# Performance work log

Hardware: AMD Instinct MI355X
Metric: run time of the kernel (lower is better)

## Reference

```python
import jax, jax.numpy as jnp
import numpy as np

B = 64          # number of scenes/graphs
OBJS = 2048     # objects per scene
N = B * OBJS    # total objects
D = 256         # representation_dim
K = 2           # num_channels


def setup_inputs() -> dict:
    key = jax.random.key(0)
    k1, k2, k3 = jax.random.split(key, 3)
    x_aggregation = jax.random.normal(k1, (N, D), dtype=jnp.float32)
    num_objs = jnp.full((B,), OBJS, dtype=jnp.int32)
    # glorot for att_shared [1, D]: fan_in + fan_out = 1 + D
    std_shared = float(np.sqrt(6.0 / (1 + D)))
    att_shared = jax.random.uniform(k2, (1, D), dtype=jnp.float32,
                                    minval=-std_shared, maxval=std_shared)
    # glorot for att_scale [K, 1]
    std_scale = float(np.sqrt(6.0 / (K + 1)))
    att_scale = jax.random.uniform(k3, (K, 1), dtype=jnp.float32,
                                   minval=-std_scale, maxval=std_scale)
    channel_bias = jnp.zeros((K, D), dtype=jnp.float32)
    return {"x_aggregation": x_aggregation, "num_objs": num_objs,
            "att_shared": att_shared, "att_scale": att_scale,
            "channel_bias": channel_bias}


def reference(x_aggregation, num_objs, att_shared, att_scale, channel_bias):
    batch_idx = jnp.repeat(jnp.arange(B), num_objs, total_repeat_length=N)  # [N]
    # scatter_mean: per-scene context features [B, D]
    seg_sum = jax.ops.segment_sum(x_aggregation, batch_idx, num_segments=B)
    counts = jnp.maximum(num_objs, 1).astype(x_aggregation.dtype)
    ctx = seg_sum / counts[:, None]
    attn_in = jax.nn.leaky_relu(x_aggregation + ctx[batch_idx], negative_slope=0.2)  # [N, D]
    # per-channel logits: ((attn_in + bias[k]) . att_shared) * scale[k]
    base = attn_in @ att_shared[0]                 # [N]
    bias_term = channel_bias @ att_shared[0]       # [K]
    logits = (base[:, None] + bias_term[None, :]) * att_scale[:, 0][None, :]  # [N, K]
    # per-channel segment softmax over objects within each scene
    m = jax.ops.segment_max(logits, batch_idx, num_segments=B)   # [B, K]
    z = jnp.exp(logits - m[batch_idx])
    s = jax.ops.segment_sum(z, batch_idx, num_segments=B)        # [B, K]
    attn_weights = z / s[batch_idx]                              # [N, K]
    # attention-weighted pooling per channel -> [B, D, K]
    weighted = x_aggregation[:, :, None] * attn_weights[:, None, :]  # [N, D, K]
    scene_features = jax.ops.segment_sum(weighted, batch_idx, num_segments=B)
    return scene_features, attn_weights
```

## Files before the change

### kernel.cpp

```cpp
#include <hip/hip_runtime.h>

#define B    64
#define OBJS 2048
#define NTOT (B * OBJS)
#define D    256
#define K    2

#define NBLK 256
#define BPS  4
#define CHF  (OBJS / BPS)
#define RPWF (CHF / 4)

#define S1   16
#define CH   (OBJS / S1)
#define RPW  (CH / 4)

#define WS_P1  0
#define WS_UP  (1024 * 256)
#define WS_ZP  (WS_UP + 1024 * 512)
#define WS_E   (WS_ZP + 1024 * 8)
#define WS_CNT (WS_E + NTOT * 2)

static __device__ __forceinline__ float lrelu02(float v) {
    return v > 0.0f ? v : 0.2f * v;
}

__global__ __launch_bounds__(256, 1) void fused_all(
        const float* __restrict__ x,
        const int* __restrict__ num_objs,
        const float* __restrict__ att_scale,
        const float* __restrict__ att_shared,
        const float* __restrict__ channel_bias,
        float* __restrict__ ws,
        float* __restrict__ out) {
    extern __shared__ float4 xbuf4[];
    __shared__ float pl[4 * 576];
    __shared__ float esm[4 * 16];
    __shared__ float sctx[D];
    __shared__ float sbt[2];
    __shared__ int   sfin;

    int blk = blockIdx.x;
    int b = blk / BPS;
    int t = threadIdx.x;
    int w = t >> 6, l = t & 63;
    int r = l & 7, sl = l >> 3;
    int row0 = blk * CHF + w * RPWF;
    int* cntA = (int*)(ws + WS_CNT);
    int* cntF = cntA + B;

    float4 kp[10][8];
    float4* xw = xbuf4 + (size_t)w * (32 * 64);
    const float* px = x + (size_t)row0 * D + 4 * l;

    float4 acc = make_float4(0.f, 0.f, 0.f, 0.f);
#pragma unroll
    for (int g = 0; g < 10; ++g) {
#pragma unroll
        for (int j = 0; j < 8; ++j) {
            float4 v = *(const float4*)(px + (size_t)(g * 8 + j) * D);
            kp[g][j] = v;
            acc.x += v.x; acc.y += v.y; acc.z += v.z; acc.w += v.w;
        }
    }
#pragma unroll
    for (int gl = 0; gl < 32; ++gl) {
        float4 v = *(const float4*)(px + (size_t)(80 + gl) * D);
        xw[gl * 64 + l] = v;
        acc.x += v.x; acc.y += v.y; acc.z += v.z; acc.w += v.w;
    }
#pragma unroll
    for (int j = 0; j < 16; ++j) {
        float4 v = *(const float4*)(px + (size_t)(112 + j) * D);
        acc.x += v.x; acc.y += v.y; acc.z += v.z; acc.w += v.w;
    }
    *(float4*)(pl + w * D + 4 * l) = acc;
    __syncthreads();
    if (t < 64) {
        float4 a = ((const float4*)(pl        ))[t];
        float4 e = ((const float4*)(pl +     D))[t];
        float4 f = ((const float4*)(pl + 2 * D))[t];
        float4 g = ((const float4*)(pl + 3 * D))[t];
        float4 s4 = make_float4(a.x + e.x + f.x + g.x, a.y + e.y + f.y + g.y,
                                a.z + e.z + f.z + g.z, a.w + e.w + f.w + g.w);
        *(float4*)(ws + WS_P1 + blk * D + 4 * t) = s4;
    }
    __syncthreads();
    if (t == 0) {
        __threadfence();
        atomicAdd(&cntA[b], 1);
        while (__hip_atomic_load(&cntA[b], __ATOMIC_RELAXED,
                                 __HIP_MEMORY_SCOPE_AGENT) < BPS)
            __builtin_amdgcn_s_sleep(2);
        __threadfence();
    }
    __syncthreads();

    {
        int cnt = num_objs[b]; if (cnt < 1) cnt = 1;
        float inv = 1.0f / (float)cnt;
        float sum = 0.f;
#pragma unroll
        for (int c = 0; c < BPS; ++c) sum += ws[WS_P1 + (b * BPS + c) * D + t];
        sctx[t] = sum * inv;
    }
    if (t < 64) {
        float4 a = ((const float4*)att_shared)[t];
#pragma unroll
        for (int k = 0; k < K; ++k) {
            float4 cb = ((const float4*)(channel_bias + k * D))[t];
            float v = a.x * cb.x + a.y * cb.y + a.z * cb.z + a.w * cb.w;
#pragma unroll
            for (int m = 32; m > 0; m >>= 1) v += __shfl_xor(v, m);
            if (t == 0) sbt[k] = v;
        }
    }
    __syncthreads();

    float4 a4   = ((const float4*)att_shared)[l];
    float4 ctx4 = *(const float4*)(sctx + 4 * l);
    float bt0 = sbt[0], bt1 = sbt[1];
    float s0 = att_scale[0], s1 = att_scale[1];

    float4 acc0 = make_float4(0.f, 0.f, 0.f, 0.f);
    float4 acc1 = make_float4(0.f, 0.f, 0.f, 0.f);
    float z0 = 0.f, z1 = 0.f;
    float e0c = 0.f, e1c = 0.f;
    float e0d = 0.f, e1d = 0.f;
    float* pw = pl  + w * 576;
    float* ew = esm + w * 16;

#define PD(V) (lrelu02((V).x + ctx4.x) * a4.x + lrelu02((V).y + ctx4.y) * a4.y \
             + lrelu02((V).z + ctx4.z) * a4.z + lrelu02((V).w + ctx4.w) * a4.w)
#define ACC(V, EA, EB) { acc0.x += (V).x * (EA); acc0.y += (V).y * (EA);      \
                         acc0.z += (V).z * (EA); acc0.w += (V).w * (EA);      \
                         acc1.x += (V).x * (EB); acc1.y += (V).y * (EB);      \
                         acc1.z += (V).z * (EB); acc1.w += (V).w * (EB); }
#define PROC_GROUP(GI, L0, L1, L2, L3, L4, L5, L6, L7) {                      \
    pw[l * 9 + 0] = PD(L0); pw[l * 9 + 1] = PD(L1);                           \
    pw[l * 9 + 2] = PD(L2); pw[l * 9 + 3] = PD(L3);                           \
    pw[l * 9 + 4] = PD(L4); pw[l * 9 + 5] = PD(L5);                           \
    pw[l * 9 + 6] = PD(L6); pw[l * 9 + 7] = PD(L7);                           \
    float tr = 0.f;                                                           \
    _Pragma("unroll")                                                         \
    for (int q = 0; q < 8; ++q) tr += pw[(sl * 8 + q) * 9 + r];               \
    tr += __shfl_xor(tr, 8);                                                  \
    tr += __shfl_xor(tr, 16);                                                 \
    tr += __shfl_xor(tr, 32);                                                 \
    float e0 = __expf((tr + bt0) * s0);                                       \
    float e1 = __expf((tr + bt1) * s1);                                       \
    if ((GI) == (l >> 3))     { e0c = e0; e1c = e1; }                         \
    if ((GI) == 8 + (l >> 3)) { e0d = e0; e1d = e1; }                         \
    if (l < 8) { ew[2 * l] = e0; ew[2 * l + 1] = e1; }                        \
    float4 E0 = *(const float4*)(ew + 0);                                     \
    float4 E1 = *(const float4*)(ew + 4);                                     \
    float4 E2 = *(const float4*)(ew + 8);                                     \
    float4 E3 = *(const float4*)(ew + 12);                                    \
    z0 += E0.x + E0.z + E1.x + E1.z + E2.x + E2.z + E3.x + E3.z;              \
    z1 += E0.y + E0.w + E1.y + E1.w + E2.y + E2.w + E3.y + E3.w;              \
    ACC(L0, E0.x, E0.y) ACC(L1, E0.z, E0.w)                                   \
    ACC(L2, E1.x, E1.y) ACC(L3, E1.z, E1.w)                                   \
    ACC(L4, E2.x, E2.y) ACC(L5, E2.z, E2.w)                                   \
    ACC(L6, E3.x, E3.y) ACC(L7, E3.z, E3.w)                                   \
}
#define PG_KP(G) PROC_GROUP(G, kp[G][0], kp[G][1], kp[G][2], kp[G][3],        \
                               kp[G][4], kp[G][5], kp[G][6], kp[G][7])

    PG_KP(0) PG_KP(1) PG_KP(2) PG_KP(3)
    float4 sa[8], sb[8];
#pragma unroll
    for (int j = 0; j < 8; ++j) sa[j] = *(const float4*)(px + (size_t)(112 + j) * D);
#pragma unroll
    for (int j = 0; j < 8; ++j) sb[j] = *(const float4*)(px + (size_t)(120 + j) * D);

    PG_KP(4) PG_KP(5) PG_KP(6) PG_KP(7) PG_KP(8) PG_KP(9)
    {
        float4 q0 = xw[0 * 64 + l], q1 = xw[1 * 64 + l], q2 = xw[2 * 64 + l],
               q3 = xw[3 * 64 + l], q4 = xw[4 * 64 + l], q5 = xw[5 * 64 + l],
               q6 = xw[6 * 64 + l], q7 = xw[7 * 64 + l];
        PROC_GROUP(10, q0, q1, q2, q3, q4, q5, q6, q7)
    }
    {
        float4 q0 = xw[8 * 64 + l], q1 = xw[9 * 64 + l], q2 = xw[10 * 64 + l],
               q3 = xw[11 * 64 + l], q4 = xw[12 * 64 + l], q5 = xw[13 * 64 + l],
               q6 = xw[14 * 64 + l], q7 = xw[15 * 64 + l];
        PROC_GROUP(11, q0, q1, q2, q3, q4, q5, q6, q7)
    }
    {
        float4 q0 = xw[16 * 64 + l], q1 = xw[17 * 64 + l], q2 = xw[18 * 64 + l],
               q3 = xw[19 * 64 + l], q4 = xw[20 * 64 + l], q5 = xw[21 * 64 + l],
               q6 = xw[22 * 64 + l], q7 = xw[23 * 64 + l];
        PROC_GROUP(12, q0, q1, q2, q3, q4, q5, q6, q7)
    }
    {
        float4 q0 = xw[24 * 64 + l], q1 = xw[25 * 64 + l], q2 = xw[26 * 64 + l],
               q3 = xw[27 * 64 + l], q4 = xw[28 * 64 + l], q5 = xw[29 * 64 + l],
               q6 = xw[30 * 64 + l], q7 = xw[31 * 64 + l];
        PROC_GROUP(13, q0, q1, q2, q3, q4, q5, q6, q7)
    }
    PROC_GROUP(14, sa[0], sa[1], sa[2], sa[3], sa[4], sa[5], sa[6], sa[7])
    PROC_GROUP(15, sb[0], sb[1], sb[2], sb[3], sb[4], sb[5], sb[6], sb[7])
#undef PG_KP
#undef PROC_GROUP
#undef ACC
#undef PD

    ((float2*)(ws + WS_E))[row0 + l]      = make_float2(e0c, e1c);
    ((float2*)(ws + WS_E))[row0 + 64 + l] = make_float2(e0d, e1d);
    if (l == 0) {
        ws[WS_ZP + blk * 8 + w * 2 + 0] = z0;
        ws[WS_ZP + blk * 8 + w * 2 + 1] = z1;
    }
    __syncthreads();
    {
        int base = w * (D * K) + l * 8;
        pl[base + 0] = acc0.x; pl[base + 1] = acc1.x;
        pl[base + 2] = acc0.y; pl[base + 3] = acc1.y;
        pl[base + 4] = acc0.z; pl[base + 5] = acc1.z;
        pl[base + 6] = acc0.w; pl[base + 7] = acc1.w;
    }
    __syncthreads();
    if (t < 128) {
        float4 a = ((const float4*)(pl       ))[t];
        float4 e = ((const float4*)(pl +  512))[t];
        float4 f = ((const float4*)(pl + 1024))[t];
        float4 g = ((const float4*)(pl + 1536))[t];
        float4 s4 = make_float4(a.x + e.x + f.x + g.x, a.y + e.y + f.y + g.y,
                                a.z + e.z + f.z + g.z, a.w + e.w + f.w + g.w);
        *(float4*)(ws + WS_UP + (size_t)blk * (D * K) + 4 * t) = s4;
    }

    __syncthreads();
    if (t == 0) {
        __threadfence();
        int old = atomicAdd(&cntF[b], 1);
        sfin = (old == BPS - 1) ? 1 : 0;
        if (sfin) __threadfence();
    }
    __syncthreads();
    if (!sfin) return;

    if (w < 2) {
        float v = (l < 16)
                ? ws[WS_ZP + (b * BPS + (l >> 2)) * 8 + (l & 3) * 2 + w] : 0.f;
        v += __shfl_xor(v, 1); v += __shfl_xor(v, 2);
        v += __shfl_xor(v, 4); v += __shfl_xor(v, 8);
        if (l == 0) sbt[w] = v;
    }
    __syncthreads();
    float zf0 = sbt[0], zf1 = sbt[1];
    float iz0 = 1.0f / zf0, iz1 = 1.0f / zf1;

#pragma unroll
    for (int j = t; j < D * K; j += 256) {
        float ssum = 0.f;
#pragma unroll
        for (int c = 0; c < BPS; ++c) ssum += ws[WS_UP + (b * BPS + c) * (D * K) + j];
        out[b * (D * K) + j] = ssum * ((j & 1) ? iz1 : iz0);
    }
    const float4* E = (const float4*)(ws + WS_E);
    float4* W = (float4*)(out + B * D * K);
#pragma unroll
    for (int i = t; i < OBJS / 2; i += 256) {
        float4 e4 = E[b * (OBJS / 2) + i];
        W[b * (OBJS / 2) + i] = make_float4(e4.x * iz0, e4.y * iz1, e4.z * iz0, e4.w * iz1);
    }
}

__global__ __launch_bounds__(256) void k1_partial(const float* __restrict__ x,
                                                  float* __restrict__ ws) {
    __shared__ float red[4 * D];
    int blk = blockIdx.x;
    int w = threadIdx.x >> 6, l = threadIdx.x & 63;
    int row0 = blk * CH + w * RPW;

    float4 acc = make_float4(0.f, 0.f, 0.f, 0.f);
    const float* px = x + (size_t)row0 * D + 4 * l;
#pragma unroll 8
    for (int j = 0; j < RPW; ++j) {
        float4 v = *(const float4*)(px + (size_t)j * D);
        acc.x += v.x; acc.y += v.y; acc.z += v.z; acc.w += v.w;
    }
    *(float4*)(red + w * D + 4 * l) = acc;
    __syncthreads();
    int t = threadIdx.x;
    if (t < 64) {
        float4 a = ((const float4*)(red        ))[t];
        float4 e = ((const float4*)(red +     D))[t];
        float4 f = ((const float4*)(red + 2 * D))[t];
        float4 g = ((const float4*)(red + 3 * D))[t];
        float4 s = make_float4(a.x + e.x + f.x + g.x, a.y + e.y + f.y + g.y,
                               a.z + e.z + f.z + g.z, a.w + e.w + f.w + g.w);
        *(float4*)(ws + WS_P1 + blk * D + 4 * t) = s;
    }
}

__global__ __launch_bounds__(256) void k2_main(const float* __restrict__ x,
                                               const int* __restrict__ num_objs,
                                               const float* __restrict__ att_scale,
                                               const float* __restrict__ att_shared,
                                               const float* __restrict__ channel_bias,
                                               float* __restrict__ ws) {
    __shared__ float pl[4 * 576];
    __shared__ float esm[4 * 16];
    __shared__ float sctx[D];
    __shared__ float sbt[2];

    int blk = blockIdx.x;
    int b = blk >> 4;
    int t = threadIdx.x;
    int w = t >> 6, l = t & 63;
    int r = l & 7, s = l >> 3;
    int row0 = blk * CH + w * RPW;

    {
        int cnt = num_objs[b]; if (cnt < 1) cnt = 1;
        float inv = 1.0f / (float)cnt;
        float sum = 0.f;
#pragma unroll
        for (int c = 0; c < S1; ++c) sum += ws[WS_P1 + (b * S1 + c) * D + t];
        sctx[t] = sum * inv;
    }
    if (t < 64) {
        float4 a = ((const float4*)att_shared)[t];
#pragma unroll
        for (int k = 0; k < K; ++k) {
            float4 cb = ((const float4*)(channel_bias + k * D))[t];
            float v = a.x * cb.x + a.y * cb.y + a.z * cb.z + a.w * cb.w;
#pragma unroll
            for (int m = 32; m > 0; m >>= 1) v += __shfl_xor(v, m);
            if (t == 0) sbt[k] = v;
        }
    }
    __syncthreads();

    float4 a4   = ((const float4*)att_shared)[l];
    float4 ctx4 = *(const float4*)(sctx + 4 * l);
    float bt0 = sbt[0], bt1 = sbt[1];
    float s0 = att_scale[0], s1 = att_scale[1];

    float4 acc0 = make_float4(0.f, 0.f, 0.f, 0.f);
    float4 acc1 = make_float4(0.f, 0.f, 0.f, 0.f);
    float z0 = 0.f, z1 = 0.f;
    float e0c = 0.f, e1c = 0.f;
    float* pw = pl  + w * 576;
    float* ew = esm + w * 16;
    const float* px = x + (size_t)row0 * D + 4 * l;

#pragma unroll
    for (int g = 0; g < 4; ++g) {
        float4 v0 = *(const float4*)(px + (size_t)(g * 8 + 0) * D);
        float4 v1 = *(const float4*)(px + (size_t)(g * 8 + 1) * D);
        float4 v2 = *(const float4*)(px + (size_t)(g * 8 + 2) * D);
        float4 v3 = *(const float4*)(px + (size_t)(g * 8 + 3) * D);
        float4 v4 = *(const float4*)(px + (size_t)(g * 8 + 4) * D);
        float4 v5 = *(const float4*)(px + (size_t)(g * 8 + 5) * D);
        float4 v6 = *(const float4*)(px + (size_t)(g * 8 + 6) * D);
        float4 v7 = *(const float4*)(px + (size_t)(g * 8 + 7) * D);

#define PDOT(V) (lrelu02((V).x + ctx4.x) * a4.x + lrelu02((V).y + ctx4.y) * a4.y \
               + lrelu02((V).z + ctx4.z) * a4.z + lrelu02((V).w + ctx4.w) * a4.w)
        pw[l * 9 + 0] = PDOT(v0); pw[l * 9 + 1] = PDOT(v1);
        pw[l * 9 + 2] = PDOT(v2); pw[l * 9 + 3] = PDOT(v3);
        pw[l * 9 + 4] = PDOT(v4); pw[l * 9 + 5] = PDOT(v5);
        pw[l * 9 + 6] = PDOT(v6); pw[l * 9 + 7] = PDOT(v7);
#undef PDOT
        float tr = 0.f;
#pragma unroll
        for (int q = 0; q < 8; ++q) tr += pw[(s * 8 + q) * 9 + r];
        tr += __shfl_xor(tr, 8);
        tr += __shfl_xor(tr, 16);
        tr += __shfl_xor(tr, 32);

        float e0 = __expf((tr + bt0) * s0);
        float e1 = __expf((tr + bt1) * s1);
        if (((l >> 3) & 3) == g) { e0c = e0; e1c = e1; }
        if (l < 8) { ew[2 * l] = e0; ew[2 * l + 1] = e1; }
        float4 E0 = *(const float4*)(ew + 0);
        float4 E1 = *(const float4*)(ew + 4);
        float4 E2 = *(const float4*)(ew + 8);
        float4 E3 = *(const float4*)(ew + 12);
        z0 += E0.x + E0.z + E1.x + E1.z + E2.x + E2.z + E3.x + E3.z;
        z1 += E0.y + E0.w + E1.y + E1.w + E2.y + E2.w + E3.y + E3.w;

#define ACC(V, EA, EB) { acc0.x += (V).x * (EA); acc0.y += (V).y * (EA);      \
                         acc0.z += (V).z * (EA); acc0.w += (V).w * (EA);      \
                         acc1.x += (V).x * (EB); acc1.y += (V).y * (EB);      \
                         acc1.z += (V).z * (EB); acc1.w += (V).w * (EB); }
        ACC(v0, E0.x, E0.y) ACC(v1, E0.z, E0.w)
        ACC(v2, E1.x, E1.y) ACC(v3, E1.z, E1.w)
        ACC(v4, E2.x, E2.y) ACC(v5, E2.z, E2.w)
        ACC(v6, E3.x, E3.y) ACC(v7, E3.z, E3.w)
#undef ACC
    }

    if (l < 32) ((float2*)(ws + WS_E))[row0 + l] = make_float2(e0c, e1c);
    if (l == 0) {
        ws[WS_ZP + blk * 8 + w * 2 + 0] = z0;
        ws[WS_ZP + blk * 8 + w * 2 + 1] = z1;
    }
    __syncthreads();
    {
        int base = w * (D * K) + l * 8;
        pl[base + 0] = acc0.x; pl[base + 1] = acc1.x;
        pl[base + 2] = acc0.y; pl[base + 3] = acc1.y;
        pl[base + 4] = acc0.z; pl[base + 5] = acc1.z;
        pl[base + 6] = acc0.w; pl[base + 7] = acc1.w;
    }
    __syncthreads();
    if (t < 128) {
        float4 a = ((const float4*)(pl       ))[t];
        float4 e = ((const float4*)(pl +  512))[t];
        float4 f = ((const float4*)(pl + 1024))[t];
        float4 g = ((const float4*)(pl + 1536))[t];
        float4 s4 = make_float4(a.x + e.x + f.x + g.x, a.y + e.y + f.y + g.y,
                                a.z + e.z + f.z + g.z, a.w + e.w + f.w + g.w);
        *(float4*)(ws + WS_UP + (size_t)blk * (D * K) + 4 * t) = s4;
    }
}

__global__ __launch_bounds__(256) void k3_final(const float* __restrict__ ws,
                                                float* __restrict__ out) {
    __shared__ float zsh[2];
    int b = blockIdx.x;
    int t = threadIdx.x;
    int w = t >> 6, l = t & 63;

    if (w < 2) {
        float v = ws[WS_ZP + (b * S1 + (l >> 2)) * 8 + (l & 3) * 2 + w];
#pragma unroll
        for (int m = 32; m > 0; m >>= 1) v += __shfl_xor(v, m);
        if (l == 0) zsh[w] = v;
    }
    __syncthreads();
    float z0 = zsh[0], z1 = zsh[1];
    float iz0 = 1.0f / z0, iz1 = 1.0f / z1;

#pragma unroll
    for (int j = t; j < D * K; j += 256) {
        float s = 0.f;
#pragma unroll
        for (int c = 0; c < S1; ++c) s += ws[WS_UP + (b * S1 + c) * (D * K) + j];
        out[b * (D * K) + j] = s * ((j & 1) ? iz1 : iz0);
    }
    const float4* E = (const float4*)(ws + WS_E);
    float4* W = (float4*)(out + B * D * K);
#pragma unroll
    for (int i = t; i < OBJS / 2; i += 256) {
        float4 e = E[b * (OBJS / 2) + i];
        W[b * (OBJS / 2) + i] = make_float4(e.x * iz0, e.y * iz1, e.z * iz0, e.w * iz1);
    }
}

extern "C" void kernel_launch(void* const* d_in, const int* in_sizes, int n_in,
                              void* d_out, int out_size, void* d_ws, size_t ws_size,
                              hipStream_t stream) {
    const float* x            = (const float*)d_in[0];
    const int*   num_objs     = (const int*)d_in[1];
    const float* att_shared   = (const float*)d_in[2];
    const float* att_scale    = (const float*)d_in[3];
    const float* channel_bias = (const float*)d_in[4];
    float* ws  = (float*)d_ws;
    float* out = (float*)d_out;

    const int DYN_LDS = 4 * 32 * 64 * (int)sizeof(float4);

    static int coop_ok = -1;
    if (coop_ok < 0) {
        (void)hipFuncSetAttribute((const void*)fused_all,
                                  hipFuncAttributeMaxDynamicSharedMemorySize,
                                  DYN_LDS);
        int nb = 0;
        hipError_t e = hipOccupancyMaxActiveBlocksPerMultiprocessor(
                &nb, fused_all, 256, DYN_LDS);
        coop_ok = (e == hipSuccess && nb >= 1) ? 1 : 0;
    }

    if (coop_ok) {
        hipMemsetAsync((char*)d_ws + sizeof(float) * (size_t)WS_CNT, 0,
                       2 * B * sizeof(int), stream);
        void* args[] = {(void*)&x, (void*)&num_objs, (void*)&att_scale,
                        (void*)&att_shared, (void*)&channel_bias,
                        (void*)&ws, (void*)&out};
        hipError_t e = hipLaunchCooperativeKernel((void*)fused_all,
                                                  dim3(NBLK), dim3(256),
                                                  args, DYN_LDS, stream);
        if (e == hipSuccess) return;
        coop_ok = 0;
    }

    k1_partial<<<B * S1, 256, 0, stream>>>(x, ws);
    k2_main<<<B * S1, 256, 0, stream>>>(x, num_objs, att_scale, att_shared,
                                        channel_bias, ws);
    k3_final<<<B, 256, 0, stream>>>(ws, out);
}
```

Before: 221.1 us.

## Split each scene across eight blocks with two blocks per CU

Doubles the grid to 512 blocks with 8 blocks per scene, halving rows per block. The register-cached tile, LDS staging buffer and tail groups shrink to match, and launch bounds now target 2 blocks per CU. The aim is to use all CUs with more resident waves, giving more memory-level parallelism on the single read-once pass over x. The cost is more partial sums and per-scene counter contention, and the cooperative path is now taken only if occupancy reports at least 2 blocks per CU.

```diff
diff --git a/kernel.cpp b/kernel.cpp
--- a/kernel.cpp
+++ b/kernel.cpp
@@ -6,8 +6,8 @@
 #define D    256
 #define K    2
 
-#define NBLK 256
-#define BPS  4
+#define NBLK 512
+#define BPS  8
 #define CHF  (OBJS / BPS)
 #define RPWF (CHF / 4)
 
@@ -25,7 +25,7 @@
     return v > 0.0f ? v : 0.2f * v;
 }
 
-__global__ __launch_bounds__(256, 1) void fused_all(
+__global__ __launch_bounds__(256, 2) void fused_all(
         const float* __restrict__ x,
         const int* __restrict__ num_objs,
         const float* __restrict__ att_scale,
@@ -49,13 +49,14 @@
     int* cntA = (int*)(ws + WS_CNT);
     int* cntF = cntA + B;
 
-    float4 kp[10][8];
-    float4* xw = xbuf4 + (size_t)w * (32 * 64);
+    float4 kp[5][8];
+    float4 sg[8];
+    float4* xw = xbuf4 + (size_t)w * (16 * 64);
     const float* px = x + (size_t)row0 * D + 4 * l;
 
     float4 acc = make_float4(0.f, 0.f, 0.f, 0.f);
 #pragma unroll
-    for (int g = 0; g < 10; ++g) {
+    for (int g = 0; g < 5; ++g) {
 #pragma unroll
         for (int j = 0; j < 8; ++j) {
             float4 v = *(const float4*)(px + (size_t)(g * 8 + j) * D);
@@ -64,14 +65,15 @@
         }
     }
 #pragma unroll
-    for (int gl = 0; gl < 32; ++gl) {
-        float4 v = *(const float4*)(px + (size_t)(80 + gl) * D);
-        xw[gl * 64 + l] = v;
+    for (int i = 0; i < 16; ++i) {
+        float4 v = *(const float4*)(px + (size_t)(40 + i) * D);
+        xw[i * 64 + l] = v;
         acc.x += v.x; acc.y += v.y; acc.z += v.z; acc.w += v.w;
     }
 #pragma unroll
-    for (int j = 0; j < 16; ++j) {
-        float4 v = *(const float4*)(px + (size_t)(112 + j) * D);
+    for (int j = 0; j < 8; ++j) {
+        float4 v = *(const float4*)(px + (size_t)(56 + j) * D);
+        sg[j] = v;
         acc.x += v.x; acc.y += v.y; acc.z += v.z; acc.w += v.w;
     }
     *(float4*)(pl + w * D + 4 * l) = acc;
@@ -126,7 +128,6 @@
     float4 acc1 = make_float4(0.f, 0.f, 0.f, 0.f);
     float z0 = 0.f, z1 = 0.f;
     float e0c = 0.f, e1c = 0.f;
-    float e0d = 0.f, e1d = 0.f;
     float* pw = pl  + w * 576;
     float* ew = esm + w * 16;
 
@@ -149,8 +150,7 @@
     tr += __shfl_xor(tr, 32);                                                 \
     float e0 = __expf((tr + bt0) * s0);                                       \
     float e1 = __expf((tr + bt1) * s1);                                       \
-    if ((GI) == (l >> 3))     { e0c = e0; e1c = e1; }                         \
-    if ((GI) == 8 + (l >> 3)) { e0d = e0; e1d = e1; }                         \
+    if ((GI) == (l >> 3)) { e0c = e0; e1c = e1; }                             \
     if (l < 8) { ew[2 * l] = e0; ew[2 * l + 1] = e1; }                        \
     float4 E0 = *(const float4*)(ew + 0);                                     \
     float4 E1 = *(const float4*)(ew + 4);                                     \
@@ -166,47 +166,26 @@
 #define PG_KP(G) PROC_GROUP(G, kp[G][0], kp[G][1], kp[G][2], kp[G][3],        \
                                kp[G][4], kp[G][5], kp[G][6], kp[G][7])
 
-    PG_KP(0) PG_KP(1) PG_KP(2) PG_KP(3)
-    float4 sa[8], sb[8];
-#pragma unroll
-    for (int j = 0; j < 8; ++j) sa[j] = *(const float4*)(px + (size_t)(112 + j) * D);
-#pragma unroll
-    for (int j = 0; j < 8; ++j) sb[j] = *(const float4*)(px + (size_t)(120 + j) * D);
-
-    PG_KP(4) PG_KP(5) PG_KP(6) PG_KP(7) PG_KP(8) PG_KP(9)
+    PG_KP(0) PG_KP(1) PG_KP(2) PG_KP(3) PG_KP(4)
     {
         float4 q0 = xw[0 * 64 + l], q1 = xw[1 * 64 + l], q2 = xw[2 * 64 + l],
                q3 = xw[3 * 64 + l], q4 = xw[4 * 64 + l], q5 = xw[5 * 64 + l],
                q6 = xw[6 * 64 + l], q7 = xw[7 * 64 + l];
-        PROC_GROUP(10, q0, q1, q2, q3, q4, q5, q6, q7)
+        PROC_GROUP(5, q0, q1, q2, q3, q4, q5, q6, q7)
     }
     {
         float4 q0 = xw[8 * 64 + l], q1 = xw[9 * 64 + l], q2 = xw[10 * 64 + l],
                q3 = xw[11 * 64 + l], q4 = xw[12 * 64 + l], q5 = xw[13 * 64 + l],
                q6 = xw[14 * 64 + l], q7 = xw[15 * 64 + l];
-        PROC_GROUP(11, q0, q1, q2, q3, q4, q5, q6, q7)
-    }
-    {
-        float4 q0 = xw[16 * 64 + l], q1 = xw[17 * 64 + l], q2 = xw[18 * 64 + l],
-               q3 = xw[19 * 64 + l], q4 = xw[20 * 64 + l], q5 = xw[21 * 64 + l],
-               q6 = xw[22 * 64 + l], q7 = xw[23 * 64 + l];
-        PROC_GROUP(12, q0, q1, q2, q3, q4, q5, q6, q7)
-    }
-    {
-        float4 q0 = xw[24 * 64 + l], q1 = xw[25 * 64 + l], q2 = xw[26 * 64 + l],
-               q3 = xw[27 * 64 + l], q4 = xw[28 * 64 + l], q5 = xw[29 * 64 + l],
-               q6 = xw[30 * 64 + l], q7 = xw[31 * 64 + l];
-        PROC_GROUP(13, q0, q1, q2, q3, q4, q5, q6, q7)
-    }
-    PROC_GROUP(14, sa[0], sa[1], sa[2], sa[3], sa[4], sa[5], sa[6], sa[7])
-    PROC_GROUP(15, sb[0], sb[1], sb[2], sb[3], sb[4], sb[5], sb[6], sb[7])
+        PROC_GROUP(6, q0, q1, q2, q3, q4, q5, q6, q7)
+    }
+    PROC_GROUP(7, sg[0], sg[1], sg[2], sg[3], sg[4], sg[5], sg[6], sg[7])
 #undef PG_KP
 #undef PROC_GROUP
 #undef ACC
 #undef PD
 
-    ((float2*)(ws + WS_E))[row0 + l]      = make_float2(e0c, e1c);
-    ((float2*)(ws + WS_E))[row0 + 64 + l] = make_float2(e0d, e1d);
+    ((float2*)(ws + WS_E))[row0 + l] = make_float2(e0c, e1c);
     if (l == 0) {
         ws[WS_ZP + blk * 8 + w * 2 + 0] = z0;
         ws[WS_ZP + blk * 8 + w * 2 + 1] = z1;
@@ -241,10 +220,11 @@
     if (!sfin) return;
 
     if (w < 2) {
-        float v = (l < 16)
+        float v = (l < 32)
                 ? ws[WS_ZP + (b * BPS + (l >> 2)) * 8 + (l & 3) * 2 + w] : 0.f;
         v += __shfl_xor(v, 1); v += __shfl_xor(v, 2);
         v += __shfl_xor(v, 4); v += __shfl_xor(v, 8);
+        v += __shfl_xor(v, 16);
         if (l == 0) sbt[w] = v;
     }
     __syncthreads();
@@ -463,7 +443,7 @@
     float* ws  = (float*)d_ws;
     float* out = (float*)d_out;
 
-    const int DYN_LDS = 4 * 32 * 64 * (int)sizeof(float4);
+    const int DYN_LDS = 4 * 16 * 64 * (int)sizeof(float4);
 
     static int coop_ok = -1;
     if (coop_ok < 0) {
@@ -473,7 +453,7 @@
         int nb = 0;
         hipError_t e = hipOccupancyMaxActiveBlocksPerMultiprocessor(
                 &nb, fused_all, 256, DYN_LDS);
-        coop_ok = (e == hipSuccess && nb >= 1) ? 1 : 0;
+        coop_ok = (e == hipSuccess && nb >= 2) ? 1 : 0;
     }
 
     if (coop_ok) {
```

After: 222.5 us. No clear change (+0.6%).
